# Optimization experiments

Measured on AMD Instinct MI355X. Metric: run time of the kernel, lower is better.

Reference implementation:

```python
import jax, jax.numpy as jnp
import numpy as np

N, D, K, MAX_ITER = 131072, 64, 512, 5


def setup_inputs() -> dict:
    key = jax.random.key(0)
    k1, k2, k3 = jax.random.split(key, 3)
    X = jax.random.normal(k1, (N, D), dtype=jnp.float32)
    centers = jax.random.normal(k2, (K, D), dtype=jnp.float32)
    repl_idx = jax.random.randint(k3, (MAX_ITER, K), 0, N, dtype=jnp.int32)
    return {"X": X, "centers": centers, "repl_idx": repl_idx}


def _assign(X, centers):
    # squared euclidean distance matrix [N, K]; argmin identical to cdist argmin
    x2 = jnp.sum(X * X, axis=1, keepdims=True)          # [N,1]
    c2 = jnp.sum(centers * centers, axis=1)             # [K]
    d2 = x2 + c2[None, :] - 2.0 * (X @ centers.T)       # [N,K]
    return jnp.argmin(d2, axis=1)


def reference(X, centers, repl_idx):
    n_clusters = centers.shape[0]
    assignments = None
    for i in range(MAX_ITER):
        assignments = _assign(X, centers)
        # scatter_mean: per-cluster sum / count (empty clusters -> 0, as torch_scatter)
        sums = jax.ops.segment_sum(X, assignments, num_segments=n_clusters)
        counts = jax.ops.segment_sum(jnp.ones((X.shape[0],), X.dtype), assignments,
                                     num_segments=n_clusters)
        new_centers = sums / jnp.maximum(counts, 1.0)[:, None]
        # re-initialize any exactly-zero entries from random data points
        new_centers_init = X[repl_idx[i]]                 # [K,D]
        new_centers = jnp.where(new_centers == 0, new_centers_init, new_centers)
        centers = new_centers
    return assignments, centers
```

## Files before the change

kernel.cpp:

```cpp
#include <hip/hip_runtime.h>

#define N_PTS 131072
#define KC    512
#define DIM   64
#define MAXIT 5
#define NCHUNK 64
#define CHUNK_PTS (N_PTS / NCHUNK)
#define FIXSCALE 1099511627776.0

typedef short v8s __attribute__((ext_vector_type(8)));
typedef float v4f __attribute__((ext_vector_type(4)));

__device__ __forceinline__ unsigned short bf16_rtne(float x) {
    unsigned int u = __float_as_uint(x);
    return (unsigned short)((u + 0x7FFFu + ((u >> 16) & 1u)) >> 16);
}
__device__ __forceinline__ float bf16_f32(unsigned short b) {
    return __uint_as_float(((unsigned int)b) << 16);
}
__device__ __forceinline__ void split3(float x, short& h, short& m, short& l) {
    unsigned short hb = bf16_rtne(x);
    float r1 = x - bf16_f32(hb);
    unsigned short mb = bf16_rtne(r1);
    float r2 = r1 - bf16_f32(mb);
    h = (short)hb; m = (short)mb; l = (short)bf16_rtne(r2);
}

__device__ __forceinline__ void gload_lds16(const unsigned short* g, void* lds) {
    __builtin_amdgcn_global_load_lds(
        (const __attribute__((address_space(1))) void*)g,
        (__attribute__((address_space(3))) void*)lds, 16, 0, 0);
}

__global__ __launch_bounds__(256) void prep_kernel(
        const float* __restrict__ C, float* __restrict__ c2out,
        unsigned short* __restrict__ Ch, unsigned short* __restrict__ Cm,
        unsigned short* __restrict__ Cl) {
    int k = blockIdx.x * 256 + threadIdx.x;
    if (k < KC) {
        float sq[DIM];
        #pragma unroll
        for (int j = 0; j < DIM; ++j) {
            float c = C[k * DIM + j];
            sq[j] = c * c;
            short h, m, l;
            split3(c, h, m, l);
            Ch[k * DIM + j] = (unsigned short)h;
            Cm[k * DIM + j] = (unsigned short)m;
            Cl[k * DIM + j] = (unsigned short)l;
        }
        #pragma unroll
        for (int st = 1; st < DIM; st <<= 1)
            #pragma unroll
            for (int j = 0; j < DIM; j += 2 * st)
                sq[j] = sq[j] + sq[j + st];
        c2out[k] = sq[0];
    }
}

__global__ __launch_bounds__(256, 4) void assign_kernel(
        const float* __restrict__ X,
        const unsigned short* __restrict__ Ch,
        const unsigned short* __restrict__ Cm,
        const unsigned short* __restrict__ Cl,
        const float* __restrict__ c2v, float* __restrict__ out_f) {
    __shared__ __align__(16) short Bt[2 * 6 * 64 * 8];
    __shared__ float c2t[KC];
    __shared__ float x2p[4][2][16][8];
    __shared__ float x2f[4][2][16];

    const int t   = threadIdx.x;
    const int wv  = t >> 6;
    const int l   = t & 63;
    const int row = l & 15;
    const int q   = l >> 4;
    const int pbase = blockIdx.x * 128 + wv * 32;

    const unsigned short* const gsrc1 =
        ((wv < 2) ? Ch : Cm) + (size_t)(row * 64 + (wv & 1) * 32 + q * 8);
    const unsigned short* const gsrc2 =
        Cl + (size_t)(row * 64 + wv * 32 + q * 8);

    v8s* const BtV = (v8s*)Bt;
    v8s* const lds1 = BtV + wv * 64;
    v8s* const lds2 = BtV + 256 + wv * 64;

    gload_lds16(gsrc1, lds1);
    if (wv < 2) gload_lds16(gsrc2, lds2);

    for (int i = t; i < KC; i += 256) c2t[i] = c2v[i];

    v8s ah[2][2], am[2][2], al[2][2];
    #pragma unroll
    for (int T = 0; T < 2; ++T) {
        const float* xr = X + (size_t)(pbase + T * 16 + row) * DIM + q * 8;
        #pragma unroll
        for (int kc = 0; kc < 2; ++kc) {
            float4 v0 = *(const float4*)(xr + kc * 32);
            float4 v1 = *(const float4*)(xr + kc * 32 + 4);
            float e[8] = { v0.x, v0.y, v0.z, v0.w, v1.x, v1.y, v1.z, v1.w };
            v8s H, M, L;
            #pragma unroll
            for (int j = 0; j < 8; ++j) {
                short hh, mm, ll;
                split3(e[j], hh, mm, ll);
                H[j] = hh; M[j] = mm; L[j] = ll;
            }
            ah[T][kc] = H; am[T][kc] = M; al[T][kc] = L;
            float s0 = e[0]*e[0], s1 = e[1]*e[1], s2 = e[2]*e[2], s3 = e[3]*e[3];
            float s4 = e[4]*e[4], s5 = e[5]*e[5], s6 = e[6]*e[6], s7 = e[7]*e[7];
            x2p[wv][T][row][kc * 4 + q] =
                ((s0 + s1) + (s2 + s3)) + ((s4 + s5) + (s6 + s7));
        }
    }
    __syncthreads();
    if (t < 128) {
        int w2 = t >> 5, T2 = (t >> 4) & 1, pt = t & 15;
        const float* P = x2p[w2][T2][pt];
        x2f[w2][T2][pt] = ((P[0] + P[1]) + (P[2] + P[3]))
                        + ((P[4] + P[5]) + (P[6] + P[7]));
    }
    __syncthreads();
    float x2x[2][4];
    #pragma unroll
    for (int T = 0; T < 2; ++T)
        #pragma unroll
        for (int r = 0; r < 4; ++r)
            x2x[T][r] = x2f[wv][T][q * 4 + r];

    float bd[2][4];
    int   bk[2][4];
    #pragma unroll
    for (int T = 0; T < 2; ++T)
        #pragma unroll
        for (int r = 0; r < 4; ++r) { bd[T][r] = 3.4e38f; bk[T][r] = 0; }

    for (int ct = 0; ct < 32; ++ct) {
        const int cur = ct & 1;
        if (ct < 31) {
            const size_t goff = (size_t)(ct + 1) * 1024;
            gload_lds16(gsrc1 + goff, lds1 + (cur ^ 1) * 384);
            if (wv < 2) gload_lds16(gsrc2 + goff, lds2 + (cur ^ 1) * 384);
        }
        v8s* const rb = BtV + cur * 384;
        v8s bh0 = rb[0 * 64 + l];
        v8s bh1 = rb[1 * 64 + l];
        v8s bm0 = rb[2 * 64 + l];
        v8s bm1 = rb[3 * 64 + l];
        v8s bl0 = rb[4 * 64 + l];
        v8s bl1 = rb[5 * 64 + l];
        float c2k = c2t[ct * 16 + row];

        #pragma unroll
        for (int T = 0; T < 2; ++T) {
            v4f acc = {0.f, 0.f, 0.f, 0.f};
            acc = __builtin_amdgcn_mfma_f32_16x16x32_bf16(ah[T][0], bh0, acc, 0, 0, 0);
            acc = __builtin_amdgcn_mfma_f32_16x16x32_bf16(ah[T][1], bh1, acc, 0, 0, 0);
            acc = __builtin_amdgcn_mfma_f32_16x16x32_bf16(am[T][0], bh0, acc, 0, 0, 0);
            acc = __builtin_amdgcn_mfma_f32_16x16x32_bf16(am[T][1], bh1, acc, 0, 0, 0);
            acc = __builtin_amdgcn_mfma_f32_16x16x32_bf16(ah[T][0], bm0, acc, 0, 0, 0);
            acc = __builtin_amdgcn_mfma_f32_16x16x32_bf16(ah[T][1], bm1, acc, 0, 0, 0);
            acc = __builtin_amdgcn_mfma_f32_16x16x32_bf16(am[T][0], bm0, acc, 0, 0, 0);
            acc = __builtin_amdgcn_mfma_f32_16x16x32_bf16(am[T][1], bm1, acc, 0, 0, 0);
            acc = __builtin_amdgcn_mfma_f32_16x16x32_bf16(al[T][0], bh0, acc, 0, 0, 0);
            acc = __builtin_amdgcn_mfma_f32_16x16x32_bf16(al[T][1], bh1, acc, 0, 0, 0);
            acc = __builtin_amdgcn_mfma_f32_16x16x32_bf16(ah[T][0], bl0, acc, 0, 0, 0);
            acc = __builtin_amdgcn_mfma_f32_16x16x32_bf16(ah[T][1], bl1, acc, 0, 0, 0);
            #pragma unroll
            for (int r = 0; r < 4; ++r) {
                float tt = x2x[T][r] + c2k;
                float d2 = fmaf(-2.0f, acc[r], tt);
                if (d2 < bd[T][r]) { bd[T][r] = d2; bk[T][r] = ct * 16 + row; }
            }
        }
        if (ct < 31) __syncthreads();
    }

    #pragma unroll
    for (int T = 0; T < 2; ++T)
        #pragma unroll
        for (int r = 0; r < 4; ++r) {
            unsigned int b = __float_as_uint(bd[T][r]);
            b = (b & 0x80000000u) ? ~b : (b | 0x80000000u);
            unsigned long long key = ((unsigned long long)b << 32)
                                   | (unsigned int)bk[T][r];
            #pragma unroll
            for (int st = 1; st <= 8; st <<= 1) {
                unsigned long long o = __shfl_xor(key, st, 64);
                if (o < key) key = o;
            }
            if (row == 0) {
                int p = pbase + T * 16 + q * 4 + r;
                out_f[p] = (float)((int)(unsigned int)key);
            }
        }
}

__global__ __launch_bounds__(1024) void accum_kernel(
        const float* __restrict__ X, const float* __restrict__ af,
        unsigned long long* __restrict__ qsums, int* __restrict__ counts) {
    __shared__ unsigned long long lsum[KC * 17];
    __shared__ int lcnt[KC];
    int slice = blockIdx.x & 3;
    int chunk = blockIdx.x >> 2;
    int p4 = threadIdx.x >> 2;
    int c4 = threadIdx.x & 3;

    for (int i = threadIdx.x; i < KC * 17; i += 1024) lsum[i] = 0ull;
    for (int i = threadIdx.x; i < KC; i += 1024) lcnt[i] = 0;
    __syncthreads();

    int base = chunk * CHUNK_PTS;
    #pragma unroll 2
    for (int it = 0; it < CHUNK_PTS / 256; ++it) {
        int n = base + it * 256 + p4;
        int a = (int)af[n];
        float4 xv = *(const float4*)(X + (size_t)n * DIM + slice * 16 + c4 * 4);
        long long q0 = (long long)llrint((double)xv.x * FIXSCALE);
        long long q1 = (long long)llrint((double)xv.y * FIXSCALE);
        long long q2 = (long long)llrint((double)xv.z * FIXSCALE);
        long long q3 = (long long)llrint((double)xv.w * FIXSCALE);
        atomicAdd(&lsum[a * 17 + c4 * 4 + 0], (unsigned long long)q0);
        atomicAdd(&lsum[a * 17 + c4 * 4 + 1], (unsigned long long)q1);
        atomicAdd(&lsum[a * 17 + c4 * 4 + 2], (unsigned long long)q2);
        atomicAdd(&lsum[a * 17 + c4 * 4 + 3], (unsigned long long)q3);
        if (slice == 0 && c4 == 0) atomicAdd(&lcnt[a], 1);
    }
    __syncthreads();

    unsigned long long* qs = qsums + (size_t)slice * (KC * 16);
    for (int i = threadIdx.x; i < KC * 16; i += 1024) {
        unsigned long long v = lsum[(i >> 4) * 17 + (i & 15)];
        if (v != 0ull) atomicAdd(&qs[i], v);
    }
    if (slice == 0)
        for (int i = threadIdx.x; i < KC; i += 1024) {
            int v = lcnt[i];
            if (v != 0) atomicAdd(&counts[i], v);
        }
}

__global__ __launch_bounds__(256) void update_kernel(
        unsigned long long* __restrict__ qsums,
        int* __restrict__ counts,
        const int* __restrict__ repl, const float* __restrict__ X,
        float* __restrict__ outC, float* __restrict__ c2v,
        unsigned short* __restrict__ Ch, unsigned short* __restrict__ Cm,
        unsigned short* __restrict__ Cl) {
    int k = blockIdx.x * 4 + (threadIdx.x >> 6);
    int d = threadIdx.x & 63;

    size_t qi = (size_t)(d >> 4) * (KC * 16) + k * 16 + (d & 15);
    long long qq = (long long)qsums[qi];
    qsums[qi] = 0ull;
    float s = (float)((double)qq * (1.0 / FIXSCALE));
    float cnt = (float)counts[k];
    float v = s / fmaxf(cnt, 1.0f);
    if (v == 0.0f) v = X[(size_t)repl[k] * DIM + d];
    outC[k * DIM + d] = v;

    short h, m, l;
    split3(v, h, m, l);
    Ch[k * DIM + d] = (unsigned short)h;
    Cm[k * DIM + d] = (unsigned short)m;
    Cl[k * DIM + d] = (unsigned short)l;

    float sq = v * v;
    #pragma unroll
    for (int st = 1; st < 64; st <<= 1)
        sq += __shfl_xor(sq, st, 64);
    if (d == 0) {
        c2v[k] = sq;
        counts[k] = 0;
    }
}

extern "C" void kernel_launch(void* const* d_in, const int* in_sizes, int n_in,
                              void* d_out, int out_size, void* d_ws, size_t ws_size,
                              hipStream_t stream) {
    const float* X    = (const float*)d_in[0];
    const float* C0   = (const float*)d_in[1];
    const int*   repl = (const int*)d_in[2];
    float* out = (float*)d_out;

    char* ws = (char*)d_ws;
    unsigned short* Ch = (unsigned short*)(ws + 0);
    unsigned short* Cm = (unsigned short*)(ws + (64 << 10));
    unsigned short* Cl = (unsigned short*)(ws + (128 << 10));
    unsigned long long* qsums = (unsigned long long*)(ws + (192 << 10));
    int*   counts = (int*)  (ws + (448 << 10));
    float* c2v    = (float*)(ws + (450 << 10));

    prep_kernel<<<2, 256, 0, stream>>>(C0, c2v, Ch, Cm, Cl);

    hipMemsetAsync(qsums, 0, KC * DIM * sizeof(unsigned long long)
                             + KC * sizeof(int), stream);

    for (int i = 0; i < MAXIT; ++i) {
        assign_kernel<<<N_PTS / 128, 256, 0, stream>>>(
            X, Ch, Cm, Cl, c2v, out);

        accum_kernel<<<NCHUNK * 4, 1024, 0, stream>>>(X, out, qsums, counts);

        update_kernel<<<KC / 4, 256, 0, stream>>>(
            qsums, counts, repl + i * KC, X, out + N_PTS, c2v, Ch, Cm, Cl);
    }
}
```

Measured before the change: 455.9 us.

## Halve points per wave in assign kernel and double occupancy target

Each wave now handles one 16-point tile instead of two, so each block covers 64 points and the grid doubles. Launch bounds raise the occupancy hint from 4 to 8 blocks per CU, which lowers register pressure and lets more waves hide latency. In exchange, each block still streams the full center set through LDS, so center-tile loads and barriers per point double and reuse of B fragments across tiles is lost.

New measurement: 498.4 us. 9.3% more time.

```diff
diff --git a/kernel.cpp b/kernel.cpp
--- a/kernel.cpp
+++ b/kernel.cpp
@@ -58,7 +58,7 @@
     }
 }
 
-__global__ __launch_bounds__(256, 4) void assign_kernel(
+__global__ __launch_bounds__(256, 8) void assign_kernel(
         const float* __restrict__ X,
         const unsigned short* __restrict__ Ch,
         const unsigned short* __restrict__ Cm,
@@ -66,15 +66,15 @@
         const float* __restrict__ c2v, float* __restrict__ out_f) {
     __shared__ __align__(16) short Bt[2 * 6 * 64 * 8];
     __shared__ float c2t[KC];
-    __shared__ float x2p[4][2][16][8];
-    __shared__ float x2f[4][2][16];
+    __shared__ float x2p[4][16][8];
+    __shared__ float x2f[4][16];
 
     const int t   = threadIdx.x;
     const int wv  = t >> 6;
     const int l   = t & 63;
     const int row = l & 15;
     const int q   = l >> 4;
-    const int pbase = blockIdx.x * 128 + wv * 32;
+    const int pbase = blockIdx.x * 64 + wv * 16;
 
     const unsigned short* const gsrc1 =
         ((wv < 2) ? Ch : Cm) + (size_t)(row * 64 + (wv & 1) * 32 + q * 8);
@@ -90,10 +90,9 @@
 
     for (int i = t; i < KC; i += 256) c2t[i] = c2v[i];
 
-    v8s ah[2][2], am[2][2], al[2][2];
-    #pragma unroll
-    for (int T = 0; T < 2; ++T) {
-        const float* xr = X + (size_t)(pbase + T * 16 + row) * DIM + q * 8;
+    v8s ah[2], am[2], al[2];
+    {
+        const float* xr = X + (size_t)(pbase + row) * DIM + q * 8;
         #pragma unroll
         for (int kc = 0; kc < 2; ++kc) {
             float4 v0 = *(const float4*)(xr + kc * 32);
@@ -106,34 +105,30 @@
                 split3(e[j], hh, mm, ll);
                 H[j] = hh; M[j] = mm; L[j] = ll;
             }
-            ah[T][kc] = H; am[T][kc] = M; al[T][kc] = L;
+            ah[kc] = H; am[kc] = M; al[kc] = L;
             float s0 = e[0]*e[0], s1 = e[1]*e[1], s2 = e[2]*e[2], s3 = e[3]*e[3];
             float s4 = e[4]*e[4], s5 = e[5]*e[5], s6 = e[6]*e[6], s7 = e[7]*e[7];
-            x2p[wv][T][row][kc * 4 + q] =
+            x2p[wv][row][kc * 4 + q] =
                 ((s0 + s1) + (s2 + s3)) + ((s4 + s5) + (s6 + s7));
         }
     }
     __syncthreads();
-    if (t < 128) {
-        int w2 = t >> 5, T2 = (t >> 4) & 1, pt = t & 15;
-        const float* P = x2p[w2][T2][pt];
-        x2f[w2][T2][pt] = ((P[0] + P[1]) + (P[2] + P[3]))
-                        + ((P[4] + P[5]) + (P[6] + P[7]));
-    }
-    __syncthreads();
-    float x2x[2][4];
-    #pragma unroll
-    for (int T = 0; T < 2; ++T)
-        #pragma unroll
-        for (int r = 0; r < 4; ++r)
-            x2x[T][r] = x2f[wv][T][q * 4 + r];
-
-    float bd[2][4];
-    int   bk[2][4];
-    #pragma unroll
-    for (int T = 0; T < 2; ++T)
-        #pragma unroll
-        for (int r = 0; r < 4; ++r) { bd[T][r] = 3.4e38f; bk[T][r] = 0; }
+    if (t < 64) {
+        int w2 = t >> 4, pt = t & 15;
+        const float* P = x2p[w2][pt];
+        x2f[w2][pt] = ((P[0] + P[1]) + (P[2] + P[3]))
+                    + ((P[4] + P[5]) + (P[6] + P[7]));
+    }
+    __syncthreads();
+    float x2x[4];
+    #pragma unroll
+    for (int r = 0; r < 4; ++r)
+        x2x[r] = x2f[wv][q * 4 + r];
+
+    float bd[4];
+    int   bk[4];
+    #pragma unroll
+    for (int r = 0; r < 4; ++r) { bd[r] = 3.4e38f; bk[r] = 0; }
 
     for (int ct = 0; ct < 32; ++ct) {
         const int cur = ct & 1;
@@ -151,49 +146,44 @@
         v8s bl1 = rb[5 * 64 + l];
         float c2k = c2t[ct * 16 + row];
 
-        #pragma unroll
-        for (int T = 0; T < 2; ++T) {
-            v4f acc = {0.f, 0.f, 0.f, 0.f};
-            acc = __builtin_amdgcn_mfma_f32_16x16x32_bf16(ah[T][0], bh0, acc, 0, 0, 0);
-            acc = __builtin_amdgcn_mfma_f32_16x16x32_bf16(ah[T][1], bh1, acc, 0, 0, 0);
-            acc = __builtin_amdgcn_mfma_f32_16x16x32_bf16(am[T][0], bh0, acc, 0, 0, 0);
-            acc = __builtin_amdgcn_mfma_f32_16x16x32_bf16(am[T][1], bh1, acc, 0, 0, 0);
-            acc = __builtin_amdgcn_mfma_f32_16x16x32_bf16(ah[T][0], bm0, acc, 0, 0, 0);
-            acc = __builtin_amdgcn_mfma_f32_16x16x32_bf16(ah[T][1], bm1, acc, 0, 0, 0);
-            acc = __builtin_amdgcn_mfma_f32_16x16x32_bf16(am[T][0], bm0, acc, 0, 0, 0);
-            acc = __builtin_amdgcn_mfma_f32_16x16x32_bf16(am[T][1], bm1, acc, 0, 0, 0);
-            acc = __builtin_amdgcn_mfma_f32_16x16x32_bf16(al[T][0], bh0, acc, 0, 0, 0);
-            acc = __builtin_amdgcn_mfma_f32_16x16x32_bf16(al[T][1], bh1, acc, 0, 0, 0);
-            acc = __builtin_amdgcn_mfma_f32_16x16x32_bf16(ah[T][0], bl0, acc, 0, 0, 0);
-            acc = __builtin_amdgcn_mfma_f32_16x16x32_bf16(ah[T][1], bl1, acc, 0, 0, 0);
-            #pragma unroll
-            for (int r = 0; r < 4; ++r) {
-                float tt = x2x[T][r] + c2k;
-                float d2 = fmaf(-2.0f, acc[r], tt);
-                if (d2 < bd[T][r]) { bd[T][r] = d2; bk[T][r] = ct * 16 + row; }
-            }
+        v4f acc = {0.f, 0.f, 0.f, 0.f};
+        acc = __builtin_amdgcn_mfma_f32_16x16x32_bf16(ah[0], bh0, acc, 0, 0, 0);
+        acc = __builtin_amdgcn_mfma_f32_16x16x32_bf16(ah[1], bh1, acc, 0, 0, 0);
+        acc = __builtin_amdgcn_mfma_f32_16x16x32_bf16(am[0], bh0, acc, 0, 0, 0);
+        acc = __builtin_amdgcn_mfma_f32_16x16x32_bf16(am[1], bh1, acc, 0, 0, 0);
+        acc = __builtin_amdgcn_mfma_f32_16x16x32_bf16(ah[0], bm0, acc, 0, 0, 0);
+        acc = __builtin_amdgcn_mfma_f32_16x16x32_bf16(ah[1], bm1, acc, 0, 0, 0);
+        acc = __builtin_amdgcn_mfma_f32_16x16x32_bf16(am[0], bm0, acc, 0, 0, 0);
+        acc = __builtin_amdgcn_mfma_f32_16x16x32_bf16(am[1], bm1, acc, 0, 0, 0);
+        acc = __builtin_amdgcn_mfma_f32_16x16x32_bf16(al[0], bh0, acc, 0, 0, 0);
+        acc = __builtin_amdgcn_mfma_f32_16x16x32_bf16(al[1], bh1, acc, 0, 0, 0);
+        acc = __builtin_amdgcn_mfma_f32_16x16x32_bf16(ah[0], bl0, acc, 0, 0, 0);
+        acc = __builtin_amdgcn_mfma_f32_16x16x32_bf16(ah[1], bl1, acc, 0, 0, 0);
+        #pragma unroll
+        for (int r = 0; r < 4; ++r) {
+            float tt = x2x[r] + c2k;
+            float d2 = fmaf(-2.0f, acc[r], tt);
+            if (d2 < bd[r]) { bd[r] = d2; bk[r] = ct * 16 + row; }
         }
         if (ct < 31) __syncthreads();
     }
 
     #pragma unroll
-    for (int T = 0; T < 2; ++T)
-        #pragma unroll
-        for (int r = 0; r < 4; ++r) {
-            unsigned int b = __float_as_uint(bd[T][r]);
-            b = (b & 0x80000000u) ? ~b : (b | 0x80000000u);
-            unsigned long long key = ((unsigned long long)b << 32)
-                                   | (unsigned int)bk[T][r];
-            #pragma unroll
-            for (int st = 1; st <= 8; st <<= 1) {
-                unsigned long long o = __shfl_xor(key, st, 64);
-                if (o < key) key = o;
-            }
-            if (row == 0) {
-                int p = pbase + T * 16 + q * 4 + r;
-                out_f[p] = (float)((int)(unsigned int)key);
-            }
-        }
+    for (int r = 0; r < 4; ++r) {
+        unsigned int b = __float_as_uint(bd[r]);
+        b = (b & 0x80000000u) ? ~b : (b | 0x80000000u);
+        unsigned long long key = ((unsigned long long)b << 32)
+                               | (unsigned int)bk[r];
+        #pragma unroll
+        for (int st = 1; st <= 8; st <<= 1) {
+            unsigned long long o = __shfl_xor(key, st, 64);
+            if (o < key) key = o;
+        }
+        if (row == 0) {
+            int p = pbase + q * 4 + r;
+            out_f[p] = (float)((int)(unsigned int)key);
+        }
+    }
 }
 
 __global__ __launch_bounds__(1024) void accum_kernel(
@@ -297,7 +287,7 @@
                              + KC * sizeof(int), stream);
 
     for (int i = 0; i < MAXIT; ++i) {
-        assign_kernel<<<N_PTS / 128, 256, 0, stream>>>(
+        assign_kernel<<<N_PTS / 64, 256, 0, stream>>>(
             X, Ch, Cm, Cl, c2v, out);
 
         accum_kernel<<<NCHUNK * 4, 1024, 0, stream>>>(X, out, qsums, counts);
```
